# Performance work log

Hardware: AMD Instinct MI355X
Metric: run time of the kernel (lower is better)

Reference implementation:

```python
import jax, jax.numpy as jnp
import numpy as np


def _sepconv1x1(x, dw, pw, b):
    # SeparableConv2D with kernel=1: depthwise 1x1 = per-channel scale, then pointwise matmul
    return jnp.einsum('nhwc,cd->nhwd', x * dw, pw) + b


def setup_inputs() -> dict:
    key = jax.random.key(0)
    ks = jax.random.split(key, 12)
    N, H, W, C_in, C_red = 4, 64, 64, 256, 64
    s = 0.05  # small init so softmax logits are well-conditioned
    return {
        'feature_maps': jax.random.normal(ks[0], (N, H, W, C_in), jnp.float32),
        'global_channel_output': jax.random.normal(ks[1], (N, H, W, C_in), jnp.float32),
        'dw_q': jax.random.normal(ks[2], (C_in,), jnp.float32) * s,
        'pw_q': jax.random.normal(ks[3], (C_in, C_red), jnp.float32) * s,
        'b_q': jnp.zeros((C_red,), jnp.float32),
        'dw_k': jax.random.normal(ks[4], (C_in,), jnp.float32) * s,
        'pw_k': jax.random.normal(ks[5], (C_in, C_red), jnp.float32) * s,
        'b_k': jnp.zeros((C_red,), jnp.float32),
        'dw_v': jax.random.normal(ks[6], (C_in,), jnp.float32) * s,
        'pw_v': jax.random.normal(ks[7], (C_in, C_red), jnp.float32) * s,
        'b_v': jnp.zeros((C_red,), jnp.float32),
        'dw_a': jax.random.normal(ks[8], (C_red,), jnp.float32) * s,
        'pw_a': jax.random.normal(ks[9], (C_red, C_in), jnp.float32) * s,
        'b_a': jnp.zeros((C_in,), jnp.float32),
    }


def reference(feature_maps, global_channel_output,
              dw_q, pw_q, b_q, dw_k, pw_k, b_k, dw_v, pw_v, b_v,
              dw_a, pw_a, b_a):
    N, H, W, _ = feature_maps.shape
    q = _sepconv1x1(feature_maps, dw_q, pw_q, b_q)  # [N,H,W,Cr]
    k = _sepconv1x1(feature_maps, dw_k, pw_k, b_k)
    v = _sepconv1x1(feature_maps, dw_v, pw_v, b_v)
    Cr = q.shape[-1]
    q = q.reshape(N, H * W, Cr)
    k = k.reshape(N, H * W, Cr)
    v = v.reshape(N, H * W, Cr)
    # tf.matmul(key, query, transpose_b=True): scores[i,j] = key_i . query_j
    scores = jnp.einsum('nic,njc->nij', k, q)  # [N,HW,HW]
    scores = jax.nn.softmax(scores, axis=-1)
    # tf.matmul(value, scores, transpose_a=True) -> [N,Cr,HW]
    att = jnp.einsum('nic,nij->ncj', v, scores)
    # faithful raw reshape (as in the original TF code) from [N,Cr,HW] to [N,H,W,Cr]
    att = att.reshape(N, H, W, Cr)
    att = _sepconv1x1(att, dw_a, pw_a, b_a)  # [N,H,W,C_in]
    return global_channel_output * att + global_channel_output
```

## Files before the change

### kernel.cpp

```cpp
#include <hip/hip_runtime.h>
#include <hip/hip_bf16.h>

typedef __attribute__((ext_vector_type(8))) __bf16 bf16x8;
typedef __attribute__((ext_vector_type(2))) __bf16 bf16x2;
typedef __attribute__((ext_vector_type(4))) float floatx4;
typedef __attribute__((ext_vector_type(4))) unsigned short us4;
typedef __attribute__((ext_vector_type(8))) unsigned short us8;
typedef __attribute__((ext_vector_type(4))) short s16x4;
typedef __attribute__((ext_vector_type(2))) unsigned int uint2v;
typedef __attribute__((ext_vector_type(4))) unsigned int uint4v;

#define MFMA16(A, B, C) __builtin_amdgcn_mfma_f32_16x16x32_bf16((A), (B), (C), 0, 0, 0)
#define MFMA1K(A, B, C) __builtin_amdgcn_mfma_f32_16x16x16bf16_1k((A), (B), (C), 0, 0, 0)

#define LOG2E 1.44269504088896340736f

#if __has_builtin(__builtin_amdgcn_exp2f)
#define EXP2F(x) __builtin_amdgcn_exp2f(x)
#else
#define EXP2F(x) exp2f(x)
#endif

static __device__ __forceinline__ unsigned short f2bfbits(float f) {
    __hip_bfloat16 h = __float2bfloat16(f);
    union { __hip_bfloat16 h; unsigned short u; } cv;
    cv.h = h;
    return cv.u;
}
static __device__ __forceinline__ unsigned int rne32(float f) {
    unsigned int u = __builtin_bit_cast(unsigned int, f);
    return u + 0x7fffu + ((u >> 16) & 1u);
}
static __device__ __forceinline__ unsigned short rne16(float f) {
    return (unsigned short)(rne32(f) >> 16);
}

#if __has_builtin(__builtin_amdgcn_cvt_pk_bf16_f32)
static __device__ __forceinline__ s16x4 pack4(float e0, float e1, float e2, float e3) {
    bf16x2 lo = __builtin_amdgcn_cvt_pk_bf16_f32(e0, e1);
    bf16x2 hi = __builtin_amdgcn_cvt_pk_bf16_f32(e2, e3);
    uint2v u = {__builtin_bit_cast(unsigned int, lo), __builtin_bit_cast(unsigned int, hi)};
    return __builtin_bit_cast(s16x4, u);
}
static __device__ __forceinline__ bf16x8 cvt8(floatx4 a, floatx4 b) {
    bf16x2 p0 = __builtin_amdgcn_cvt_pk_bf16_f32(a[0], a[1]);
    bf16x2 p1 = __builtin_amdgcn_cvt_pk_bf16_f32(a[2], a[3]);
    bf16x2 p2 = __builtin_amdgcn_cvt_pk_bf16_f32(b[0], b[1]);
    bf16x2 p3 = __builtin_amdgcn_cvt_pk_bf16_f32(b[2], b[3]);
    uint4v u = {__builtin_bit_cast(unsigned int, p0), __builtin_bit_cast(unsigned int, p1),
                __builtin_bit_cast(unsigned int, p2), __builtin_bit_cast(unsigned int, p3)};
    return __builtin_bit_cast(bf16x8, u);
}
#else
static __device__ __forceinline__ s16x4 pack4(float e0, float e1, float e2, float e3) {
    unsigned int pa = __builtin_amdgcn_perm(rne32(e1), rne32(e0), 0x07060302u);
    unsigned int pb = __builtin_amdgcn_perm(rne32(e3), rne32(e2), 0x07060302u);
    uint2v u = {pa, pb};
    return __builtin_bit_cast(s16x4, u);
}
static __device__ __forceinline__ bf16x8 cvt8(floatx4 a, floatx4 b) {
    us8 u;
#pragma unroll
    for (int i = 0; i < 4; i++) { u[i] = rne16(a[i]); u[4 + i] = rne16(b[i]); }
    return __builtin_bit_cast(bf16x8, u);
}
#endif

static __device__ __forceinline__ bf16x8 load_bf8(const __hip_bfloat16* p) {
    return *reinterpret_cast<const bf16x8*>(p);
}
static __device__ __forceinline__ float bf2f(unsigned short u) {
    unsigned int w = ((unsigned int)u) << 16;
    return __builtin_bit_cast(float, w);
}

static __device__ __forceinline__ void gld16(const void* g, void* l) {
    __builtin_amdgcn_global_load_lds(
        (const __attribute__((address_space(1))) unsigned int*)g,
        (__attribute__((address_space(3))) unsigned int*)l, 16, 0, 0);
}


__global__ __launch_bounds__(256) void proj_qkv(
    const float* __restrict__ x,
    const float* __restrict__ dwq, const float* __restrict__ pwq,
    const float* __restrict__ dwk, const float* __restrict__ pwk,
    const float* __restrict__ dwv, const float* __restrict__ pwv,
    const float* __restrict__ bqp, const float* __restrict__ bkp,
    const float* __restrict__ bvp,
    __hip_bfloat16* __restrict__ qf, __hip_bfloat16* __restrict__ kf,
    __hip_bfloat16* __restrict__ vf)
{
    __shared__ __hip_bfloat16 wle[16384];
    int b = blockIdx.x;
    int p = b >> 8;
    int tg = b & 255;
    int tid = threadIdx.x;

    const float* dw = (p == 0) ? dwq : ((p == 1) ? dwk : dwv);
    const float* pw = (p == 0) ? pwq : ((p == 1) ? pwk : pwv);
    float scale = (p == 1) ? LOG2E : 1.0f;

    {
        float dwc = dw[tid];
#pragma unroll
        for (int k = 0; k < 64; k++) {
            int idx = (k * 256 + tid) ^ ((k & 7) << 3);
            wle[idx] = __float2bfloat16(dwc * pw[tid * 64 + k] * scale);
        }
    }
    __syncthreads();

    int wv = tid >> 6;
    int wid = tg * 4 + wv;
    int lane = tid & 63;
    int l15 = lane & 15, quad = lane >> 4;

    floatx4 acc[4];
#pragma unroll
    for (int t = 0; t < 4; t++) acc[t] = (floatx4){0.f, 0.f, 0.f, 0.f};

    const float* xrow = x + (wid * 16 + l15) * 256 + quad * 8;
#pragma unroll
    for (int ks = 0; ks < 8; ks++) {
        floatx4 xa = *reinterpret_cast<const floatx4*>(xrow + ks * 32);
        floatx4 xb = *reinterpret_cast<const floatx4*>(xrow + ks * 32 + 4);
        bf16x8 a = cvt8(xa, xb);
#pragma unroll
        for (int t = 0; t < 4; t++) {
            int j0 = ((t * 16 + l15) * 256 + ks * 32 + quad * 8) ^ ((l15 & 7) << 3);
            bf16x8 bfr = *reinterpret_cast<const bf16x8*>(&wle[j0]);
            acc[t] = MFMA16(a, bfr, acc[t]);
        }
    }
    if (p < 2) {
        __hip_bfloat16* dst = (p == 0) ? qf : kf;
        const float* bias = (p == 0) ? bqp : bkp;
        float bscale = (p == 1) ? LOG2E : 1.0f;
#pragma unroll
        for (int t = 0; t < 4; t++) {
            float bsv = bias[t * 16 + l15] * bscale;
            int off0 = wid * 1024 + (t >> 1) * 512 +
                       (((((t & 1) << 1) | (l15 >> 3)) * 16 + quad * 4) * 8) + (l15 & 7);
#pragma unroll
            for (int r = 0; r < 4; r++)
                dst[off0 + r * 8] = __float2bfloat16(acc[t][r] + bsv);
        }
    } else {
#pragma unroll
        for (int t = 0; t < 4; t++) {
            float bsv = bvp[t * 16 + l15];
            us4 pk;
#pragma unroll
            for (int r = 0; r < 4; r++) pk[r] = f2bfbits(acc[t][r] + bsv);
            *reinterpret_cast<us4*>(vf + (wid * 4 + t) * 256 + lane * 4) = pk;
        }
    }
}

#define P1STEP(B0, B1, B2, B3) do {                                        \
    floatx4 z = (floatx4){0.f, 0.f, 0.f, 0.f};                             \
    floatx4 s0 = MFMA16(a1, (B1), MFMA16(a0, (B0), z));                    \
    floatx4 s1 = MFMA16(a1, (B3), MFMA16(a0, (B2), z));                    \
    floatx4 s2 = MFMA16(a3, (B1), MFMA16(a2, (B0), z));                    \
    floatx4 s3 = MFMA16(a3, (B3), MFMA16(a2, (B2), z));                    \
    floatx4 s4 = MFMA16(a5, (B1), MFMA16(a4, (B0), z));                    \
    floatx4 s5 = MFMA16(a5, (B3), MFMA16(a4, (B2), z));                    \
    floatx4 s6 = MFMA16(a7, (B1), MFMA16(a6, (B0), z));                    \
    floatx4 s7 = MFMA16(a7, (B3), MFMA16(a6, (B2), z));                    \
    _Pragma("unroll")                                                      \
    for (int r = 0; r < 4; r++) {                                          \
        ls0[r] += EXP2F(s0[r]) + EXP2F(s1[r]);                             \
        ls1[r] += EXP2F(s2[r]) + EXP2F(s3[r]);                             \
        ls2[r] += EXP2F(s4[r]) + EXP2F(s5[r]);                             \
        ls3[r] += EXP2F(s6[r]) + EXP2F(s7[r]);                             \
    }                                                                      \
} while (0)

__global__ __launch_bounds__(256) void pass1_rl(
    const __hip_bfloat16* __restrict__ qf, const __hip_bfloat16* __restrict__ kf,
    float* __restrict__ rl)
{
    int itg0 = blockIdx.x * 4;
    int n = itg0 >> 8;
    int jw = threadIdx.x >> 6;
    int lane = threadIdx.x & 63;
    int l15 = lane & 15, quad = lane >> 4;

    const __hip_bfloat16* kp = kf + itg0 * 1024 + lane * 8;
    bf16x8 a0 = load_bf8(kp);
    bf16x8 a1 = load_bf8(kp + 512);
    bf16x8 a2 = load_bf8(kp + 1024);
    bf16x8 a3 = load_bf8(kp + 1536);
    bf16x8 a4 = load_bf8(kp + 2048);
    bf16x8 a5 = load_bf8(kp + 2560);
    bf16x8 a6 = load_bf8(kp + 3072);
    bf16x8 a7 = load_bf8(kp + 3584);

    floatx4 ls0 = (floatx4){0.f, 0.f, 0.f, 0.f};
    floatx4 ls1 = (floatx4){0.f, 0.f, 0.f, 0.f};
    floatx4 ls2 = (floatx4){0.f, 0.f, 0.f, 0.f};
    floatx4 ls3 = (floatx4){0.f, 0.f, 0.f, 0.f};
    const __hip_bfloat16* qp0 = qf + (n * 256 + jw * 64) * 1024 + lane * 8;

    bf16x8 s0b0 = load_bf8(qp0);
    bf16x8 s0b1 = load_bf8(qp0 + 512);
    bf16x8 s0b2 = load_bf8(qp0 + 1024);
    bf16x8 s0b3 = load_bf8(qp0 + 1536);
    bf16x8 s1b0 = load_bf8(qp0 + 2048);
    bf16x8 s1b1 = load_bf8(qp0 + 2560);
    bf16x8 s1b2 = load_bf8(qp0 + 3072);
    bf16x8 s1b3 = load_bf8(qp0 + 3584);

    for (int it = 0; it < 32; it += 2) {
        bf16x8 n0 = load_bf8(qp0 + 4096);
        bf16x8 n1 = load_bf8(qp0 + 4608);
        bf16x8 n2 = load_bf8(qp0 + 5120);
        bf16x8 n3 = load_bf8(qp0 + 5632);
        P1STEP(s0b0, s0b1, s0b2, s0b3);
        s0b0 = n0; s0b1 = n1; s0b2 = n2; s0b3 = n3;
        bf16x8 m0 = load_bf8(qp0 + 6144);
        bf16x8 m1 = load_bf8(qp0 + 6656);
        bf16x8 m2 = load_bf8(qp0 + 7168);
        bf16x8 m3 = load_bf8(qp0 + 7680);
        P1STEP(s1b0, s1b1, s1b2, s1b3);
        s1b0 = m0; s1b1 = m1; s1b2 = m2; s1b3 = m3;
        qp0 += 4096;
    }
#pragma unroll
    for (int m = 1; m < 16; m <<= 1) {
#pragma unroll
        for (int r = 0; r < 4; r++) {
            ls0[r] += __shfl_xor(ls0[r], m, 64);
            ls1[r] += __shfl_xor(ls1[r], m, 64);
            ls2[r] += __shfl_xor(ls2[r], m, 64);
            ls3[r] += __shfl_xor(ls3[r], m, 64);
        }
    }
    __shared__ float red[4][64];
    if (l15 == 0) {
#pragma unroll
        for (int r = 0; r < 4; r++) {
            red[jw][quad * 4 + r]      = ls0[r];
            red[jw][16 + quad * 4 + r] = ls1[r];
            red[jw][32 + quad * 4 + r] = ls2[r];
            red[jw][48 + quad * 4 + r] = ls3[r];
        }
    }
    __syncthreads();
    if (threadIdx.x < 64) {
        float tot = red[0][threadIdx.x] + red[1][threadIdx.x] +
                    red[2][threadIdx.x] + red[3][threadIdx.x];
        rl[itg0 * 16 + threadIdx.x] = 1.0f / tot;
    }
}

#define P2STEP(KA, KB, V0, V1, V2, V3, RLQ) do {                               \
    floatx4 z = (floatx4){0.f, 0.f, 0.f, 0.f};                                 \
    floatx4 s0 = MFMA16((KB), bq0b, MFMA16((KA), bq0a, z));                    \
    floatx4 s1 = MFMA16((KB), bq1b, MFMA16((KA), bq1a, z));                    \
    floatx4 s2 = MFMA16((KB), bq2b, MFMA16((KA), bq2a, z));                    \
    floatx4 s3 = MFMA16((KB), bq3b, MFMA16((KA), bq3a, z));                    \
    s16x4 p0 = pack4(EXP2F(s0[0]) * (RLQ)[0], EXP2F(s0[1]) * (RLQ)[1],         \
                     EXP2F(s0[2]) * (RLQ)[2], EXP2F(s0[3]) * (RLQ)[3]);        \
    s16x4 p1 = pack4(EXP2F(s1[0]) * (RLQ)[0], EXP2F(s1[1]) * (RLQ)[1],         \
                     EXP2F(s1[2]) * (RLQ)[2], EXP2F(s1[3]) * (RLQ)[3]);        \
    s16x4 p2 = pack4(EXP2F(s2[0]) * (RLQ)[0], EXP2F(s2[1]) * (RLQ)[1],         \
                     EXP2F(s2[2]) * (RLQ)[2], EXP2F(s2[3]) * (RLQ)[3]);        \
    s16x4 p3 = pack4(EXP2F(s3[0]) * (RLQ)[0], EXP2F(s3[1]) * (RLQ)[1],         \
                     EXP2F(s3[2]) * (RLQ)[2], EXP2F(s3[3]) * (RLQ)[3]);        \
    acc0[0] = MFMA1K(p0, (V0), acc0[0]);                                       \
    acc1[0] = MFMA1K(p1, (V0), acc1[0]);                                       \
    acc2[0] = MFMA1K(p2, (V0), acc2[0]);                                       \
    acc3[0] = MFMA1K(p3, (V0), acc3[0]);                                       \
    acc0[1] = MFMA1K(p0, (V1), acc0[1]);                                       \
    acc1[1] = MFMA1K(p1, (V1), acc1[1]);                                       \
    acc2[1] = MFMA1K(p2, (V1), acc2[1]);                                       \
    acc3[1] = MFMA1K(p3, (V1), acc3[1]);                                       \
    acc0[2] = MFMA1K(p0, (V2), acc0[2]);                                       \
    acc1[2] = MFMA1K(p1, (V2), acc1[2]);                                       \
    acc2[2] = MFMA1K(p2, (V2), acc2[2]);                                       \
    acc3[2] = MFMA1K(p3, (V2), acc3[2]);                                       \
    acc0[3] = MFMA1K(p0, (V3), acc0[3]);                                       \
    acc1[3] = MFMA1K(p1, (V3), acc1[3]);                                       \
    acc2[3] = MFMA1K(p2, (V3), acc2[3]);                                       \
    acc3[3] = MFMA1K(p3, (V3), acc3[3]);                                       \
} while (0)

__global__ __launch_bounds__(512) void pass2_att(
    const __hip_bfloat16* __restrict__ qf, const __hip_bfloat16* __restrict__ kf,
    const __hip_bfloat16* __restrict__ vf, const float* __restrict__ rl,
    unsigned short* __restrict__ attp)
{
    __shared__ char ldsbuf[2][8192];
    __shared__ float rl_lds[512];
    int b = blockIdx.x;
    int ih = b & 7;
    int jgrp = (b >> 3) & 7;
    int n = b >> 6;
    int tid = threadIdx.x;
    int w = tid >> 6;
    int lane = tid & 63;
    int l15 = lane & 15, quad = lane >> 4;
    int jt0 = jgrp * 32 + w * 4;

    int it0 = n * 256 + ih * 32;

    if (tid < 128)
        *reinterpret_cast<floatx4*>(&rl_lds[tid * 4]) =
            *reinterpret_cast<const floatx4*>(&rl[it0 * 16 + tid * 4]);

    const __hip_bfloat16* qp = qf + (n * 256 + jt0) * 1024 + lane * 8;
    bf16x8 bq0a = load_bf8(qp);
    bf16x8 bq0b = load_bf8(qp + 512);
    bf16x8 bq1a = load_bf8(qp + 1024);
    bf16x8 bq1b = load_bf8(qp + 1536);
    bf16x8 bq2a = load_bf8(qp + 2048);
    bf16x8 bq2b = load_bf8(qp + 2560);
    bf16x8 bq3a = load_bf8(qp + 3072);
    bf16x8 bq3b = load_bf8(qp + 3584);

    floatx4 acc0[4], acc1[4], acc2[4], acc3[4];
#pragma unroll
    for (int t = 0; t < 4; t++) {
        acc0[t] = (floatx4){0.f, 0.f, 0.f, 0.f};
        acc1[t] = (floatx4){0.f, 0.f, 0.f, 0.f};
        acc2[t] = (floatx4){0.f, 0.f, 0.f, 0.f};
        acc3[t] = (floatx4){0.f, 0.f, 0.f, 0.f};
    }

    const char* gbase = (w < 4) ? (const char*)(kf + it0 * 1024)
                                : (const char*)(vf + it0 * 1024);
    const char* gw = gbase + ((w >> 1) & 1) * 2048 + (w & 1) * 1024 + lane * 16;
    char* lw0 = &ldsbuf[0][w * 1024];
    char* lw1 = &ldsbuf[1][w * 1024];

    gld16(gw, lw0);
    __syncthreads();

    int cur = 0;
    for (int ph = 0; ph < 16; ph++) {
        if (ph < 15)
            gld16(gw + (ph + 1) * 4096, cur ? lw0 : lw1);
        const char* base = ldsbuf[cur];
#pragma unroll
        for (int t = 0; t < 2; t++) {
            bf16x8 a0 = *reinterpret_cast<const bf16x8*>(base + t * 2048 + lane * 16);
            bf16x8 a1 = *reinterpret_cast<const bf16x8*>(base + t * 2048 + 1024 + lane * 16);
            const char* vb = base + 4096 + t * 2048 + lane * 8;
            s16x4 v0 = *reinterpret_cast<const s16x4*>(vb);
            s16x4 v1 = *reinterpret_cast<const s16x4*>(vb + 512);
            s16x4 v2 = *reinterpret_cast<const s16x4*>(vb + 1024);
            s16x4 v3 = *reinterpret_cast<const s16x4*>(vb + 1536);
            floatx4 rlq = *reinterpret_cast<const floatx4*>(
                &rl_lds[(ph * 2 + t) * 16 + quad * 4]);
            P2STEP(a0, a1, v0, v1, v2, v3, rlq);
        }
        __syncthreads();
        cur ^= 1;
    }
    unsigned short* op0 = attp + ih * 1048576;
#pragma unroll
    for (int t = 0; t < 4; t++) {
        s16x4 k0 = pack4(acc0[t][0], acc0[t][1], acc0[t][2], acc0[t][3]);
        s16x4 k1 = pack4(acc1[t][0], acc1[t][1], acc1[t][2], acc1[t][3]);
        s16x4 k2 = pack4(acc2[t][0], acc2[t][1], acc2[t][2], acc2[t][3]);
        s16x4 k3 = pack4(acc3[t][0], acc3[t][1], acc3[t][2], acc3[t][3]);
        unsigned short* op = op0 + (n * 64 + t * 16 + l15) * 4096 + jt0 * 16 + quad * 4;
        *reinterpret_cast<s16x4*>(op) = k0;
        *reinterpret_cast<s16x4*>(op + 16) = k1;
        *reinterpret_cast<s16x4*>(op + 32) = k2;
        *reinterpret_cast<s16x4*>(op + 48) = k3;
    }
}

template<int NPART>
__global__ __launch_bounds__(256) void final_out(
    const unsigned short* __restrict__ attp, const float* __restrict__ gco,
    const float* __restrict__ dwa, const float* __restrict__ pwa,
    const float* __restrict__ ba, float* __restrict__ out)
{
    int b = blockIdx.x;
    int n = b >> 9;
    int hh = (b >> 3) & 63;
    int w0 = (b & 7) << 3;
    __shared__ float g[512];
    int tid = threadIdx.x;
    const unsigned short* ap = attp + (n * 64 + hh) * 4096 + w0 * 64;
    {
        int jj0 = tid * 2;
        float v0 = 0.f, v1 = 0.f;
#pragma unroll
        for (int ph = 0; ph < NPART; ph++) {
            unsigned int u = *reinterpret_cast<const unsigned int*>(ap + ph * 1048576 + jj0);
            v0 += bf2f((unsigned short)(u & 0xffffu));
            v1 += bf2f((unsigned short)(u >> 16));
        }
        g[jj0] = v0 * dwa[jj0 & 63];
        g[jj0 + 1] = v1 * dwa[(jj0 + 1) & 63];
    }
    __syncthreads();
    float acc[8];
#pragma unroll
    for (int w = 0; w < 8; w++) acc[w] = 0.f;
    for (int cc = 0; cc < 64; cc++) {
        float p = pwa[cc * 256 + tid];
#pragma unroll
        for (int w = 0; w < 8; w++) acc[w] += g[w * 64 + cc] * p;
    }
    float bb = ba[tid];
#pragma unroll
    for (int w = 0; w < 8; w++) {
        int pos = (n * 64 + hh) * 64 + w0 + w;
        float gv = gco[pos * 256 + tid];
        out[pos * 256 + tid] = gv * (acc[w] + bb) + gv;
    }
}

extern "C" void kernel_launch(void* const* d_in, const int* in_sizes, int n_in,
                              void* d_out, int out_size, void* d_ws, size_t ws_size,
                              hipStream_t stream) {
    const float* x   = (const float*)d_in[0];
    const float* gco = (const float*)d_in[1];
    const float* dwq = (const float*)d_in[2];
    const float* pwq = (const float*)d_in[3];
    const float* bq  = (const float*)d_in[4];
    const float* dwk = (const float*)d_in[5];
    const float* pwk = (const float*)d_in[6];
    const float* bk  = (const float*)d_in[7];
    const float* dwv = (const float*)d_in[8];
    const float* pwv = (const float*)d_in[9];
    const float* bv  = (const float*)d_in[10];
    const float* dwa = (const float*)d_in[11];
    const float* pwa = (const float*)d_in[12];
    const float* ba  = (const float*)d_in[13];
    float* out = (float*)d_out;

    char* ws = (char*)d_ws;
    __hip_bfloat16* qf  = (__hip_bfloat16*)(ws + 98304);
    __hip_bfloat16* kf  = (__hip_bfloat16*)(ws + 2195456);
    __hip_bfloat16* vf  = (__hip_bfloat16*)(ws + 4292608);
    float*          rlb = (float*)(ws + 6389760);
    unsigned short* attp = (unsigned short*)(ws + 8486912);

    proj_qkv<<<768, 256, 0, stream>>>(x, dwq, pwq, dwk, pwk, dwv, pwv,
                                      bq, bk, bv, qf, kf, vf);
    pass1_rl<<<256, 256, 0, stream>>>(qf, kf, rlb);
    pass2_att<<<256, 512, 0, stream>>>(qf, kf, vf, rlb, attp);
    final_out<8><<<2048, 256, 0, stream>>>(attp, gco, dwa, pwa, ba, out);
}
```

Before: 184.5 us.

## Split pass1 softmax row-sum kernel into more blocks with wider j-split

The pass1 row-sum kernel now gives each block 32 key rows instead of 64 and uses 8 waves instead of 4. Each wave covers 512 query columns instead of 1024. The grid doubles to 512 blocks of 512 threads. This spreads the exp-sum work over more blocks and waves so more CUs stay busy and each wave has a shorter serial loop. In exchange, every block reloads the query data for its batch, which doubles Q traffic, and the cross-wave reduction grows.

```diff
diff --git a/kernel.cpp b/kernel.cpp
--- a/kernel.cpp
+++ b/kernel.cpp
@@ -160,28 +160,22 @@
 
 #define P1STEP(B0, B1, B2, B3) do {                                        \
     floatx4 z = (floatx4){0.f, 0.f, 0.f, 0.f};                             \
-    floatx4 s0 = MFMA16(a1, (B1), MFMA16(a0, (B0), z));                    \
-    floatx4 s1 = MFMA16(a1, (B3), MFMA16(a0, (B2), z));                    \
-    floatx4 s2 = MFMA16(a3, (B1), MFMA16(a2, (B0), z));                    \
-    floatx4 s3 = MFMA16(a3, (B3), MFMA16(a2, (B2), z));                    \
-    floatx4 s4 = MFMA16(a5, (B1), MFMA16(a4, (B0), z));                    \
-    floatx4 s5 = MFMA16(a5, (B3), MFMA16(a4, (B2), z));                    \
-    floatx4 s6 = MFMA16(a7, (B1), MFMA16(a6, (B0), z));                    \
-    floatx4 s7 = MFMA16(a7, (B3), MFMA16(a6, (B2), z));                    \
+    floatx4 sA0 = MFMA16(a1, (B1), MFMA16(a0, (B0), z));                   \
+    floatx4 sA1 = MFMA16(a1, (B3), MFMA16(a0, (B2), z));                   \
+    floatx4 sB0 = MFMA16(a3, (B1), MFMA16(a2, (B0), z));                   \
+    floatx4 sB1 = MFMA16(a3, (B3), MFMA16(a2, (B2), z));                   \
     _Pragma("unroll")                                                      \
     for (int r = 0; r < 4; r++) {                                          \
-        ls0[r] += EXP2F(s0[r]) + EXP2F(s1[r]);                             \
-        ls1[r] += EXP2F(s2[r]) + EXP2F(s3[r]);                             \
-        ls2[r] += EXP2F(s4[r]) + EXP2F(s5[r]);                             \
-        ls3[r] += EXP2F(s6[r]) + EXP2F(s7[r]);                             \
+        lsA[r] += EXP2F(sA0[r]) + EXP2F(sA1[r]);                           \
+        lsB[r] += EXP2F(sB0[r]) + EXP2F(sB1[r]);                           \
     }                                                                      \
 } while (0)
 
-__global__ __launch_bounds__(256) void pass1_rl(
+__global__ __launch_bounds__(512) void pass1_rl(
     const __hip_bfloat16* __restrict__ qf, const __hip_bfloat16* __restrict__ kf,
     float* __restrict__ rl)
 {
-    int itg0 = blockIdx.x * 4;
+    int itg0 = blockIdx.x * 2;
     int n = itg0 >> 8;
     int jw = threadIdx.x >> 6;
     int lane = threadIdx.x & 63;
@@ -192,16 +186,10 @@
     bf16x8 a1 = load_bf8(kp + 512);
     bf16x8 a2 = load_bf8(kp + 1024);
     bf16x8 a3 = load_bf8(kp + 1536);
-    bf16x8 a4 = load_bf8(kp + 2048);
-    bf16x8 a5 = load_bf8(kp + 2560);
-    bf16x8 a6 = load_bf8(kp + 3072);
-    bf16x8 a7 = load_bf8(kp + 3584);
-
-    floatx4 ls0 = (floatx4){0.f, 0.f, 0.f, 0.f};
-    floatx4 ls1 = (floatx4){0.f, 0.f, 0.f, 0.f};
-    floatx4 ls2 = (floatx4){0.f, 0.f, 0.f, 0.f};
-    floatx4 ls3 = (floatx4){0.f, 0.f, 0.f, 0.f};
-    const __hip_bfloat16* qp0 = qf + (n * 256 + jw * 64) * 1024 + lane * 8;
+
+    floatx4 lsA = (floatx4){0.f, 0.f, 0.f, 0.f};
+    floatx4 lsB = (floatx4){0.f, 0.f, 0.f, 0.f};
+    const __hip_bfloat16* qp0 = qf + (n * 256 + jw * 32) * 1024 + lane * 8;
 
     bf16x8 s0b0 = load_bf8(qp0);
     bf16x8 s0b1 = load_bf8(qp0 + 512);
@@ -212,7 +200,7 @@
     bf16x8 s1b2 = load_bf8(qp0 + 3072);
     bf16x8 s1b3 = load_bf8(qp0 + 3584);
 
-    for (int it = 0; it < 32; it += 2) {
+    for (int it = 0; it < 16; it += 2) {
         bf16x8 n0 = load_bf8(qp0 + 4096);
         bf16x8 n1 = load_bf8(qp0 + 4608);
         bf16x8 n2 = load_bf8(qp0 + 5120);
@@ -231,26 +219,23 @@
     for (int m = 1; m < 16; m <<= 1) {
 #pragma unroll
         for (int r = 0; r < 4; r++) {
-            ls0[r] += __shfl_xor(ls0[r], m, 64);
-            ls1[r] += __shfl_xor(ls1[r], m, 64);
-            ls2[r] += __shfl_xor(ls2[r], m, 64);
-            ls3[r] += __shfl_xor(ls3[r], m, 64);
-        }
-    }
-    __shared__ float red[4][64];
+            lsA[r] += __shfl_xor(lsA[r], m, 64);
+            lsB[r] += __shfl_xor(lsB[r], m, 64);
+        }
+    }
+    __shared__ float red[8][32];
     if (l15 == 0) {
 #pragma unroll
         for (int r = 0; r < 4; r++) {
-            red[jw][quad * 4 + r]      = ls0[r];
-            red[jw][16 + quad * 4 + r] = ls1[r];
-            red[jw][32 + quad * 4 + r] = ls2[r];
-            red[jw][48 + quad * 4 + r] = ls3[r];
+            red[jw][quad * 4 + r] = lsA[r];
+            red[jw][16 + quad * 4 + r] = lsB[r];
         }
     }
     __syncthreads();
-    if (threadIdx.x < 64) {
-        float tot = red[0][threadIdx.x] + red[1][threadIdx.x] +
-                    red[2][threadIdx.x] + red[3][threadIdx.x];
+    if (threadIdx.x < 32) {
+        float tot = 0.f;
+#pragma unroll
+        for (int w = 0; w < 8; w++) tot += red[w][threadIdx.x];
         rl[itg0 * 16 + threadIdx.x] = 1.0f / tot;
     }
 }
@@ -445,7 +430,7 @@
 
     proj_qkv<<<768, 256, 0, stream>>>(x, dwq, pwq, dwk, pwk, dwv, pwv,
                                       bq, bk, bv, qf, kf, vf);
-    pass1_rl<<<256, 256, 0, stream>>>(qf, kf, rlb);
+    pass1_rl<<<512, 512, 0, stream>>>(qf, kf, rlb);
     pass2_att<<<256, 512, 0, stream>>>(qf, kf, vf, rlb, attp);
     final_out<8><<<2048, 256, 0, stream>>>(attp, gco, dwa, pwa, ba, out);
 }
```

New measurement: 167.2 us. -9.4%, faster.
